# Performance work log

Measured on AMD Instinct MI355X. Metric: run time of the kernel, lower is better.

The kernel has to match this reference:

```python
import jax, jax.numpy as jnp
import numpy as np

NUM_GROUPS = 131072
GROUP_SIZE = 3          # trigenic interaction queries (Dango)
HIDDEN = 128
NUM_HEADS = 4
HEAD_DIM = HIDDEN // NUM_HEADS
NUM_LAYERS = 2


def setup_inputs() -> dict:
    key = jax.random.key(0)
    ks = jax.random.split(key, 16)
    N = NUM_GROUPS * GROUP_SIZE
    H, L = HIDDEN, NUM_LAYERS
    s = 1.0 / np.sqrt(H)
    inp = {
        "gene_embeddings": jax.random.normal(ks[0], (N, H), dtype=jnp.float32),
        "batch": jnp.repeat(jnp.arange(NUM_GROUPS, dtype=jnp.int64), GROUP_SIZE),
        # static embedding Linear
        "Ws": jax.random.uniform(ks[1], (H, H), jnp.float32, -s, s),
        "bs": jnp.zeros((H,), jnp.float32),
        # per-layer attention projections, stacked over layers
        "Wq": jax.random.uniform(ks[2], (L, H, H), jnp.float32, -s, s),
        "bq": jnp.zeros((L, H), jnp.float32),
        "Wk": jax.random.uniform(ks[3], (L, H, H), jnp.float32, -s, s),
        "bk": jnp.zeros((L, H), jnp.float32),
        "Wv": jax.random.uniform(ks[4], (L, H, H), jnp.float32, -s, s),
        "bv": jnp.zeros((L, H), jnp.float32),
        "Wo": jax.random.uniform(ks[5], (L, H, H), jnp.float32, -s, s),
        "bo": jnp.zeros((L, H), jnp.float32),
        # ReZero params, init 0.01 as in module
        "beta": jnp.full((L,), 0.01, jnp.float32),
        # prediction layer (xavier_uniform)
        "Wp": jax.random.uniform(ks[6], (H, 1), jnp.float32, -np.sqrt(6.0 / (H + 1)), np.sqrt(6.0 / (H + 1))),
        "bp": jnp.zeros((1,), jnp.float32),
    }
    return inp


def _attention_layer(xg, Wq, bq, Wk, bk, Wv, bv, Wo, bo, beta):
    # xg: [G, S, H] block-diagonal groups; exclude-self masked MHA + ReZero.
    G, S, H = xg.shape
    q = (xg @ Wq + bq).reshape(G, S, NUM_HEADS, HEAD_DIM)
    k = (xg @ Wk + bk).reshape(G, S, NUM_HEADS, HEAD_DIM)
    v = (xg @ Wv + bv).reshape(G, S, NUM_HEADS, HEAD_DIM)
    scores = jnp.einsum("gqhd,gkhd->ghqk", q, k) / np.sqrt(HEAD_DIM)
    self_mask = jnp.eye(S, dtype=bool)  # exclude self-attention
    scores = jnp.where(self_mask, -jnp.inf, scores)
    attn = jax.nn.softmax(scores, axis=-1)
    attn = jnp.nan_to_num(attn, nan=0.0)  # torch.nan_to_num parity
    out = jnp.einsum("ghqk,gkhd->gqhd", attn, v).reshape(G, S, H)
    out = out @ Wo + bo
    return xg + beta * out  # ReZero residual (dropout: eval mode identity)


def reference(gene_embeddings, batch, Ws, bs, Wq, bq, Wk, bk, Wv, bv, Wo, bo, beta, Wp, bp):
    N, H = gene_embeddings.shape
    G = N // GROUP_SIZE
    static = jax.nn.relu(gene_embeddings @ Ws + bs)  # static embedding MLP
    dyn = gene_embeddings.reshape(G, GROUP_SIZE, H)
    for i in range(NUM_LAYERS):
        dyn = _attention_layer(dyn, Wq[i], bq[i], Wk[i], bk[i],
                               Wv[i], bv[i], Wo[i], bo[i], beta[i])
    dyn = dyn.reshape(N, H)
    diff_sq = (dyn - static) ** 2
    gene_scores = (diff_sq @ Wp + bp).squeeze(-1)  # [N]
    # scatter_mean over batch ids
    sums = jax.ops.segment_sum(gene_scores, batch, num_segments=G)
    cnts = jax.ops.segment_sum(jnp.ones_like(gene_scores), batch, num_segments=G)
    interaction_scores = sums / jnp.maximum(cnts, 1.0)
    return interaction_scores[:, None]  # [G, 1]
```

## Files before the change

### kernel.cpp

```cpp
#include <hip/hip_runtime.h>
#include <hip/hip_bf16.h>

#define NGROUPS 131072
#define H 128
#define SG 3
#define NHEADS 4
#define HD 32
#define GB 16
#define MR 48
#define NT 512
#define BP 136
#define NLAYERS 2

typedef unsigned short u16;
typedef unsigned int u32;
typedef __bf16 bf16x8 __attribute__((ext_vector_type(8)));
typedef float floatx4 __attribute__((ext_vector_type(4)));

__device__ __forceinline__ float bf2f_lo(u32 u) {
  union { u32 i; float f; } c; c.i = u << 16; return c.f;
}
__device__ __forceinline__ float bf2f_hi(u32 u) {
  union { u32 i; float f; } c; c.i = u & 0xffff0000u; return c.f;
}
__device__ __forceinline__ u32 f2bf2(float a, float b) {
  __hip_bfloat162 h = __float22bfloat162_rn(make_float2(a, b));
  union { __hip_bfloat162 h; u32 u; } c; c.h = h; return c.u;
}
__device__ __forceinline__ u16 f2bf(float f) {
  union { float f; u32 i; } c; c.f = f;
  u32 x = c.i; x += 0x7fffu + ((x >> 16) & 1u);
  return (u16)(x >> 16);
}

__global__ void wconv_kernel(const float* __restrict__ Ws, const float* __restrict__ Wq,
                             const float* __restrict__ Wk, const float* __restrict__ Wv,
                             const float* __restrict__ Wo, u16* __restrict__ wt) {
  int idx = blockIdx.x * 256 + threadIdx.x;
  int slot = idx >> 14;
  int rem = idx & 16383;
  int n = rem >> 7, k = rem & 127;
  const float* src;
  if (slot == 0) src = Ws;
  else {
    int l = (slot - 1) >> 2, t = (slot - 1) & 3;
    const float* base = (t == 0) ? Wq : (t == 1) ? Wk : (t == 2) ? Wv : Wo;
    src = base + l * (H * H);
  }
  wt[idx] = f2bf(src[k * H + n]);
}

template <int NP>
__device__ __forceinline__ void multi_proj(const u16* __restrict__ lds,
                                           const u16* __restrict__ w0,
                                           floatx4 acc[NP][3], int m0, int qi, int wrow) {
#pragma unroll
  for (int p = 0; p < NP; p++)
#pragma unroll
    for (int nt = 0; nt < 3; nt++)
      acc[p][nt] = (floatx4){0.f, 0.f, 0.f, 0.f};
#pragma unroll
  for (int kk = 0; kk < 4; kk++) {
    bf16x8 b[3];
#pragma unroll
    for (int nt = 0; nt < 3; nt++)
      b[nt] = *reinterpret_cast<const bf16x8*>(lds + (nt * 16 + m0) * BP + kk * 32 + qi * 8);
#pragma unroll
    for (int p = 0; p < NP; p++) {
      bf16x8 a = *reinterpret_cast<const bf16x8*>(w0 + (size_t)p * H * H + wrow * H + kk * 32 + qi * 8);
#pragma unroll
      for (int nt = 0; nt < 3; nt++)
        acc[p][nt] = __builtin_amdgcn_mfma_f32_16x16x32_bf16(a, b[nt], acc[p][nt], 0, 0, 0);
    }
  }
}

__device__ __forceinline__ void store_proj(u16* __restrict__ buf, const floatx4 acc[3],
                                           float4 b4, int m0, int colb) {
#pragma unroll
  for (int nt = 0; nt < 3; nt++) {
    uint2 pp;
    pp.x = f2bf2(acc[nt][0] + b4.x, acc[nt][1] + b4.y);
    pp.y = f2bf2(acc[nt][2] + b4.z, acc[nt][3] + b4.w);
    *reinterpret_cast<uint2*>(buf + (nt * 16 + m0) * BP + colb) = pp;
  }
}

__global__ void __launch_bounds__(NT)
__attribute__((amdgpu_waves_per_eu(4)))
dango_kernel(const float* __restrict__ x, const u16* __restrict__ wt,
             const float* __restrict__ bs, const float* __restrict__ bq,
             const float* __restrict__ bk, const float* __restrict__ bv,
             const float* __restrict__ bo, const float* __restrict__ beta,
             const float* __restrict__ Wp, const float* __restrict__ bp,
             float* __restrict__ out)
{
  __shared__ __align__(16) u16 xbf[MR][BP];
  __shared__ __align__(16) u16 qbuf[MR][BP];
  __shared__ __align__(16) u16 kbuf[MR][BP];
  __shared__ __align__(16) u16 vbuf[MR][BP];
  __shared__ float attnw[GB][NHEADS][SG][2];
  __shared__ float rowsc[MR][9];

  const int tid = threadIdx.x;
  const int lane = tid & 63;
  const int wave = tid >> 6;
  const int m0 = lane & 15;
  const int qi = lane >> 4;
  const int colb = wave * 16 + qi * 4;
  const int wrow = wave * 16 + m0;
  const int row0 = blockIdx.x * MR;

  float xdyn[3][4];
  u32 statpk[3][2];

#pragma unroll
  for (int nt = 0; nt < 3; nt++) {
    int row = nt * 16 + m0;
    float4 v = *reinterpret_cast<const float4*>(x + (size_t)(row0 + row) * H + colb);
    xdyn[nt][0] = v.x; xdyn[nt][1] = v.y; xdyn[nt][2] = v.z; xdyn[nt][3] = v.w;
    uint2 pp; pp.x = f2bf2(v.x, v.y); pp.y = f2bf2(v.z, v.w);
    *reinterpret_cast<uint2*>(&xbf[row][colb]) = pp;
  }
  __syncthreads();

  {
    floatx4 acc[4][3];
    multi_proj<4>(&xbf[0][0], wt, acc, m0, qi, wrow);
    {
      float4 b4 = *reinterpret_cast<const float4*>(bs + colb);
#pragma unroll
      for (int nt = 0; nt < 3; nt++) {
        statpk[nt][0] = f2bf2(fmaxf(acc[0][nt][0] + b4.x, 0.f), fmaxf(acc[0][nt][1] + b4.y, 0.f));
        statpk[nt][1] = f2bf2(fmaxf(acc[0][nt][2] + b4.z, 0.f), fmaxf(acc[0][nt][3] + b4.w, 0.f));
      }
    }
    store_proj(&qbuf[0][0], acc[1], *reinterpret_cast<const float4*>(bq + colb), m0, colb);
    store_proj(&kbuf[0][0], acc[2], *reinterpret_cast<const float4*>(bk + colb), m0, colb);
    store_proj(&vbuf[0][0], acc[3], *reinterpret_cast<const float4*>(bv + colb), m0, colb);
  }
  __syncthreads();

  for (int l = 0; l < NLAYERS; l++) {
    if (tid < GB * NHEADS * SG) {
      int g = tid / (NHEADS * SG);
      int rem = tid % (NHEADS * SG);
      int h = rem / SG;
      int i = rem % SG;
      int j0 = (i == 0) ? 1 : 0;
      int j1 = (i == 2) ? 1 : 2;
      const uint4* qp  = reinterpret_cast<const uint4*>(&qbuf[g * 3 + i][h * HD]);
      const uint4* k0p = reinterpret_cast<const uint4*>(&kbuf[g * 3 + j0][h * HD]);
      const uint4* k1p = reinterpret_cast<const uint4*>(&kbuf[g * 3 + j1][h * HD]);
      float s0 = 0.f, s1 = 0.f;
#pragma unroll
      for (int c = 0; c < 4; c++) {
        uint4 qu = qp[c], u0 = k0p[c], u1 = k1p[c];
        u32 qs[4] = {qu.x, qu.y, qu.z, qu.w};
        u32 a0[4] = {u0.x, u0.y, u0.z, u0.w};
        u32 a1[4] = {u1.x, u1.y, u1.z, u1.w};
#pragma unroll
        for (int e = 0; e < 4; e++) {
          float ql = bf2f_lo(qs[e]), qh = bf2f_hi(qs[e]);
          s0 += ql * bf2f_lo(a0[e]) + qh * bf2f_hi(a0[e]);
          s1 += ql * bf2f_lo(a1[e]) + qh * bf2f_hi(a1[e]);
        }
      }
      s0 *= 0.17677669529663687f;
      s1 *= 0.17677669529663687f;
      float mx = fmaxf(s0, s1);
      float e0 = __expf(s0 - mx), e1 = __expf(s1 - mx);
      float inv = 1.f / (e0 + e1);
      attnw[g][h][i][0] = e0 * inv;
      attnw[g][h][i][1] = e1 * inv;
    }
    __syncthreads();

    for (int ch = tid; ch < MR * 16; ch += NT) {
      int r = ch >> 4, c0 = (ch & 15) << 3;
      int g = r / 3, i = r - g * 3, h = c0 >> 5;
      int j0 = (i == 0) ? 1 : 0;
      int j1 = (i == 2) ? 1 : 2;
      float a0 = attnw[g][h][i][0], a1 = attnw[g][h][i][1];
      uint4 v0 = *reinterpret_cast<const uint4*>(&vbuf[g * 3 + j0][c0]);
      uint4 v1 = *reinterpret_cast<const uint4*>(&vbuf[g * 3 + j1][c0]);
      u32 w0[4] = {v0.x, v0.y, v0.z, v0.w};
      u32 w1[4] = {v1.x, v1.y, v1.z, v1.w};
      u32 oo[4];
#pragma unroll
      for (int e = 0; e < 4; e++) {
        float lo = a0 * bf2f_lo(w0[e]) + a1 * bf2f_lo(w1[e]);
        float hi = a0 * bf2f_hi(w0[e]) + a1 * bf2f_hi(w1[e]);
        oo[e] = f2bf2(lo, hi);
      }
      uint4 o; o.x = oo[0]; o.y = oo[1]; o.z = oo[2]; o.w = oo[3];
      *reinterpret_cast<uint4*>(&qbuf[r][c0]) = o;
    }
    __syncthreads();

    {
      floatx4 acc[1][3];
      multi_proj<1>(&qbuf[0][0], wt + (size_t)(1 + l * 4 + 3) * H * H, acc, m0, qi, wrow);
      float4 b4 = *reinterpret_cast<const float4*>(bo + l * H + colb);
      const float betal = beta[l];
#pragma unroll
      for (int nt = 0; nt < 3; nt++) {
        xdyn[nt][0] += betal * (acc[0][nt][0] + b4.x);
        xdyn[nt][1] += betal * (acc[0][nt][1] + b4.y);
        xdyn[nt][2] += betal * (acc[0][nt][2] + b4.z);
        xdyn[nt][3] += betal * (acc[0][nt][3] + b4.w);
      }
    }

    if (l + 1 < NLAYERS) {
#pragma unroll
      for (int nt = 0; nt < 3; nt++) {
        uint2 pp;
        pp.x = f2bf2(xdyn[nt][0], xdyn[nt][1]);
        pp.y = f2bf2(xdyn[nt][2], xdyn[nt][3]);
        *reinterpret_cast<uint2*>(&xbf[nt * 16 + m0][colb]) = pp;
      }
      __syncthreads();

      floatx4 acc[3][3];
      multi_proj<3>(&xbf[0][0], wt + (size_t)(1 + (l + 1) * 4) * H * H, acc, m0, qi, wrow);
      store_proj(&qbuf[0][0], acc[0], *reinterpret_cast<const float4*>(bq + (l + 1) * H + colb), m0, colb);
      store_proj(&kbuf[0][0], acc[1], *reinterpret_cast<const float4*>(bk + (l + 1) * H + colb), m0, colb);
      store_proj(&vbuf[0][0], acc[2], *reinterpret_cast<const float4*>(bv + (l + 1) * H + colb), m0, colb);
      __syncthreads();
    }
  }

  float4 wp4 = *reinterpret_cast<const float4*>(Wp + colb);
  float rsum[3];
#pragma unroll
  for (int nt = 0; nt < 3; nt++) {
    float d0 = xdyn[nt][0] - bf2f_lo(statpk[nt][0]);
    float d1 = xdyn[nt][1] - bf2f_hi(statpk[nt][0]);
    float d2 = xdyn[nt][2] - bf2f_lo(statpk[nt][1]);
    float d3 = xdyn[nt][3] - bf2f_hi(statpk[nt][1]);
    rsum[nt] = d0 * d0 * wp4.x + d1 * d1 * wp4.y + d2 * d2 * wp4.z + d3 * d3 * wp4.w;
  }
#pragma unroll
  for (int nt = 0; nt < 3; nt++) {
    rsum[nt] += __shfl_xor(rsum[nt], 16, 64);
    rsum[nt] += __shfl_xor(rsum[nt], 32, 64);
  }
  if (qi == 0) {
#pragma unroll
    for (int nt = 0; nt < 3; nt++)
      rowsc[nt * 16 + m0][wave] = rsum[nt];
  }
  __syncthreads();
  if (tid < GB) {
    float s = 0.f;
#pragma unroll
    for (int i = 0; i < SG; i++) {
      int row = tid * 3 + i;
#pragma unroll
      for (int w = 0; w < 8; w++) s += rowsc[row][w];
    }
    out[blockIdx.x * GB + tid] = s * (1.f / 3.f) + bp[0];
  }
}

extern "C" void kernel_launch(void* const* d_in, const int* in_sizes, int n_in,
                              void* d_out, int out_size, void* d_ws, size_t ws_size,
                              hipStream_t stream) {
  const float* x    = (const float*)d_in[0];
  const float* Ws   = (const float*)d_in[2];
  const float* bs   = (const float*)d_in[3];
  const float* Wq   = (const float*)d_in[4];
  const float* bq   = (const float*)d_in[5];
  const float* Wk   = (const float*)d_in[6];
  const float* bk   = (const float*)d_in[7];
  const float* Wv   = (const float*)d_in[8];
  const float* bv   = (const float*)d_in[9];
  const float* Wo   = (const float*)d_in[10];
  const float* bo   = (const float*)d_in[11];
  const float* beta = (const float*)d_in[12];
  const float* Wp   = (const float*)d_in[13];
  const float* bp   = (const float*)d_in[14];
  float* out = (float*)d_out;
  u16* wt = (u16*)d_ws;

  wconv_kernel<<<576, 256, 0, stream>>>(Ws, Wq, Wk, Wv, Wo, wt);
  dango_kernel<<<NGROUPS / GB, NT, 0, stream>>>(x, wt, bs, bq, bk, bv, bo, beta, Wp, bp, out);
}
```

Baseline: 577.4 us.

## Cut LDS and registers by reusing buffers and staging the residual in bf16

Removes the separate V buffer: the V projection is now computed after the softmax into qbuf, and the attention output is written into kbuf. The attention-weight and row-score arrays share one overlay array. The fp32 residual no longer lives in registers; it is read back from the bf16 xbf buffer each layer, and waves_per_eu is raised from 4 to 6. The aim is to cut LDS and register use so more blocks fit per CU. The cost is an extra barrier and a serialized V projection, plus some precision loss because the residual is rounded to bf16 between layers.

```diff
diff --git a/kernel.cpp b/kernel.cpp
--- a/kernel.cpp
+++ b/kernel.cpp
@@ -87,7 +87,7 @@
 }
 
 __global__ void __launch_bounds__(NT)
-__attribute__((amdgpu_waves_per_eu(4)))
+__attribute__((amdgpu_waves_per_eu(6)))
 dango_kernel(const float* __restrict__ x, const u16* __restrict__ wt,
              const float* __restrict__ bs, const float* __restrict__ bq,
              const float* __restrict__ bk, const float* __restrict__ bv,
@@ -98,9 +98,9 @@
   __shared__ __align__(16) u16 xbf[MR][BP];
   __shared__ __align__(16) u16 qbuf[MR][BP];
   __shared__ __align__(16) u16 kbuf[MR][BP];
-  __shared__ __align__(16) u16 vbuf[MR][BP];
-  __shared__ float attnw[GB][NHEADS][SG][2];
-  __shared__ float rowsc[MR][9];
+  __shared__ __align__(16) float ovl[MR * 9];
+#define ATTNW(g, h, i, p) ovl[((((g) * NHEADS + (h)) * SG + (i)) << 1) + (p)]
+#define ROWSC(r, w) ovl[(r) * 9 + (w)]
 
   const int tid = threadIdx.x;
   const int lane = tid & 63;
@@ -111,33 +111,33 @@
   const int wrow = wave * 16 + m0;
   const int row0 = blockIdx.x * MR;
 
-  float xdyn[3][4];
   u32 statpk[3][2];
+  float dynf[3][4];
 
 #pragma unroll
   for (int nt = 0; nt < 3; nt++) {
     int row = nt * 16 + m0;
     float4 v = *reinterpret_cast<const float4*>(x + (size_t)(row0 + row) * H + colb);
-    xdyn[nt][0] = v.x; xdyn[nt][1] = v.y; xdyn[nt][2] = v.z; xdyn[nt][3] = v.w;
     uint2 pp; pp.x = f2bf2(v.x, v.y); pp.y = f2bf2(v.z, v.w);
     *reinterpret_cast<uint2*>(&xbf[row][colb]) = pp;
   }
   __syncthreads();
 
   {
-    floatx4 acc[4][3];
-    multi_proj<4>(&xbf[0][0], wt, acc, m0, qi, wrow);
+    floatx4 acc2[2][3];
+    multi_proj<2>(&xbf[0][0], wt, acc2, m0, qi, wrow);
     {
       float4 b4 = *reinterpret_cast<const float4*>(bs + colb);
 #pragma unroll
       for (int nt = 0; nt < 3; nt++) {
-        statpk[nt][0] = f2bf2(fmaxf(acc[0][nt][0] + b4.x, 0.f), fmaxf(acc[0][nt][1] + b4.y, 0.f));
-        statpk[nt][1] = f2bf2(fmaxf(acc[0][nt][2] + b4.z, 0.f), fmaxf(acc[0][nt][3] + b4.w, 0.f));
-      }
-    }
-    store_proj(&qbuf[0][0], acc[1], *reinterpret_cast<const float4*>(bq + colb), m0, colb);
-    store_proj(&kbuf[0][0], acc[2], *reinterpret_cast<const float4*>(bk + colb), m0, colb);
-    store_proj(&vbuf[0][0], acc[3], *reinterpret_cast<const float4*>(bv + colb), m0, colb);
+        statpk[nt][0] = f2bf2(fmaxf(acc2[0][nt][0] + b4.x, 0.f), fmaxf(acc2[0][nt][1] + b4.y, 0.f));
+        statpk[nt][1] = f2bf2(fmaxf(acc2[0][nt][2] + b4.z, 0.f), fmaxf(acc2[0][nt][3] + b4.w, 0.f));
+      }
+    }
+    store_proj(&qbuf[0][0], acc2[1], *reinterpret_cast<const float4*>(bq + colb), m0, colb);
+    floatx4 acc1[1][3];
+    multi_proj<1>(&xbf[0][0], wt + (size_t)2 * H * H, acc1, m0, qi, wrow);
+    store_proj(&kbuf[0][0], acc1[0], *reinterpret_cast<const float4*>(bk + colb), m0, colb);
   }
   __syncthreads();
 
@@ -171,8 +171,15 @@
       float mx = fmaxf(s0, s1);
       float e0 = __expf(s0 - mx), e1 = __expf(s1 - mx);
       float inv = 1.f / (e0 + e1);
-      attnw[g][h][i][0] = e0 * inv;
-      attnw[g][h][i][1] = e1 * inv;
+      ATTNW(g, h, i, 0) = e0 * inv;
+      ATTNW(g, h, i, 1) = e1 * inv;
+    }
+    __syncthreads();
+
+    {
+      floatx4 acc1[1][3];
+      multi_proj<1>(&xbf[0][0], wt + (size_t)(1 + l * 4 + 2) * H * H, acc1, m0, qi, wrow);
+      store_proj(&qbuf[0][0], acc1[0], *reinterpret_cast<const float4*>(bv + l * H + colb), m0, colb);
     }
     __syncthreads();
 
@@ -181,9 +188,9 @@
       int g = r / 3, i = r - g * 3, h = c0 >> 5;
       int j0 = (i == 0) ? 1 : 0;
       int j1 = (i == 2) ? 1 : 2;
-      float a0 = attnw[g][h][i][0], a1 = attnw[g][h][i][1];
-      uint4 v0 = *reinterpret_cast<const uint4*>(&vbuf[g * 3 + j0][c0]);
-      uint4 v1 = *reinterpret_cast<const uint4*>(&vbuf[g * 3 + j1][c0]);
+      float a0 = ATTNW(g, h, i, 0), a1 = ATTNW(g, h, i, 1);
+      uint4 v0 = *reinterpret_cast<const uint4*>(&qbuf[g * 3 + j0][c0]);
+      uint4 v1 = *reinterpret_cast<const uint4*>(&qbuf[g * 3 + j1][c0]);
       u32 w0[4] = {v0.x, v0.y, v0.z, v0.w};
       u32 w1[4] = {v1.x, v1.y, v1.z, v1.w};
       u32 oo[4];
@@ -194,39 +201,38 @@
         oo[e] = f2bf2(lo, hi);
       }
       uint4 o; o.x = oo[0]; o.y = oo[1]; o.z = oo[2]; o.w = oo[3];
-      *reinterpret_cast<uint4*>(&qbuf[r][c0]) = o;
+      *reinterpret_cast<uint4*>(&kbuf[r][c0]) = o;
     }
     __syncthreads();
 
     {
-      floatx4 acc[1][3];
-      multi_proj<1>(&qbuf[0][0], wt + (size_t)(1 + l * 4 + 3) * H * H, acc, m0, qi, wrow);
+      floatx4 acc1[1][3];
+      multi_proj<1>(&kbuf[0][0], wt + (size_t)(1 + l * 4 + 3) * H * H, acc1, m0, qi, wrow);
       float4 b4 = *reinterpret_cast<const float4*>(bo + l * H + colb);
       const float betal = beta[l];
 #pragma unroll
       for (int nt = 0; nt < 3; nt++) {
-        xdyn[nt][0] += betal * (acc[0][nt][0] + b4.x);
-        xdyn[nt][1] += betal * (acc[0][nt][1] + b4.y);
-        xdyn[nt][2] += betal * (acc[0][nt][2] + b4.z);
-        xdyn[nt][3] += betal * (acc[0][nt][3] + b4.w);
+        int row = nt * 16 + m0;
+        uint2 pp = *reinterpret_cast<const uint2*>(&xbf[row][colb]);
+        float r0 = bf2f_lo(pp.x) + betal * (acc1[0][nt][0] + b4.x);
+        float r1 = bf2f_hi(pp.x) + betal * (acc1[0][nt][1] + b4.y);
+        float r2 = bf2f_lo(pp.y) + betal * (acc1[0][nt][2] + b4.z);
+        float r3 = bf2f_hi(pp.y) + betal * (acc1[0][nt][3] + b4.w);
+        if (l + 1 < NLAYERS) {
+          uint2 np; np.x = f2bf2(r0, r1); np.y = f2bf2(r2, r3);
+          *reinterpret_cast<uint2*>(&xbf[row][colb]) = np;
+        } else {
+          dynf[nt][0] = r0; dynf[nt][1] = r1; dynf[nt][2] = r2; dynf[nt][3] = r3;
+        }
       }
     }
 
     if (l + 1 < NLAYERS) {
-#pragma unroll
-      for (int nt = 0; nt < 3; nt++) {
-        uint2 pp;
-        pp.x = f2bf2(xdyn[nt][0], xdyn[nt][1]);
-        pp.y = f2bf2(xdyn[nt][2], xdyn[nt][3]);
-        *reinterpret_cast<uint2*>(&xbf[nt * 16 + m0][colb]) = pp;
-      }
       __syncthreads();
-
-      floatx4 acc[3][3];
-      multi_proj<3>(&xbf[0][0], wt + (size_t)(1 + (l + 1) * 4) * H * H, acc, m0, qi, wrow);
-      store_proj(&qbuf[0][0], acc[0], *reinterpret_cast<const float4*>(bq + (l + 1) * H + colb), m0, colb);
-      store_proj(&kbuf[0][0], acc[1], *reinterpret_cast<const float4*>(bk + (l + 1) * H + colb), m0, colb);
-      store_proj(&vbuf[0][0], acc[2], *reinterpret_cast<const float4*>(bv + (l + 1) * H + colb), m0, colb);
+      floatx4 acc2[2][3];
+      multi_proj<2>(&xbf[0][0], wt + (size_t)(1 + (l + 1) * 4) * H * H, acc2, m0, qi, wrow);
+      store_proj(&qbuf[0][0], acc2[0], *reinterpret_cast<const float4*>(bq + (l + 1) * H + colb), m0, colb);
+      store_proj(&kbuf[0][0], acc2[1], *reinterpret_cast<const float4*>(bk + (l + 1) * H + colb), m0, colb);
       __syncthreads();
     }
   }
@@ -235,10 +241,10 @@
   float rsum[3];
 #pragma unroll
   for (int nt = 0; nt < 3; nt++) {
-    float d0 = xdyn[nt][0] - bf2f_lo(statpk[nt][0]);
-    float d1 = xdyn[nt][1] - bf2f_hi(statpk[nt][0]);
-    float d2 = xdyn[nt][2] - bf2f_lo(statpk[nt][1]);
-    float d3 = xdyn[nt][3] - bf2f_hi(statpk[nt][1]);
+    float d0 = dynf[nt][0] - bf2f_lo(statpk[nt][0]);
+    float d1 = dynf[nt][1] - bf2f_hi(statpk[nt][0]);
+    float d2 = dynf[nt][2] - bf2f_lo(statpk[nt][1]);
+    float d3 = dynf[nt][3] - bf2f_hi(statpk[nt][1]);
     rsum[nt] = d0 * d0 * wp4.x + d1 * d1 * wp4.y + d2 * d2 * wp4.z + d3 * d3 * wp4.w;
   }
 #pragma unroll
@@ -249,7 +255,7 @@
   if (qi == 0) {
 #pragma unroll
     for (int nt = 0; nt < 3; nt++)
-      rowsc[nt * 16 + m0][wave] = rsum[nt];
+      ROWSC(nt * 16 + m0, wave) = rsum[nt];
   }
   __syncthreads();
   if (tid < GB) {
@@ -258,7 +264,7 @@
     for (int i = 0; i < SG; i++) {
       int row = tid * 3 + i;
 #pragma unroll
-      for (int w = 0; w < 8; w++) s += rowsc[row][w];
+      for (int w = 0; w < 8; w++) s += ROWSC(row, w);
     }
     out[blockIdx.x * GB + tid] = s * (1.f / 3.f) + bp[0];
   }
```

Result: slower. 599.0 us (+3.7%).
